# Optimization experiments

Measured on AMD Instinct MI355X. Metric: run time of the kernel, lower is better.

The kernel has to match this reference:

```python
import jax, jax.numpy as jnp
import numpy as np

N_NODES = 50000
N_EDGES = 1600000
NFEAT = 256
NHID = 32
HEADS = 8
NCLASS = 2
NEG_SLOPE = 0.2  # DGL GATConv default


def gat_layer(x, src, dst, W, al, ar, b, num_nodes):
    """DGL-style GATConv layer.
    x: [N, in], W: [in, H*F], al/ar: [H, F], b: [H*F].
    Returns [N, H*F].
    """
    H, F = al.shape
    feat = (x @ W).reshape(num_nodes, H, F)          # [N, H, F]
    el = jnp.einsum('nhf,hf->nh', feat, al)          # [N, H]
    er = jnp.einsum('nhf,hf->nh', feat, ar)          # [N, H]
    e = jax.nn.leaky_relu(el[src] + er[dst], NEG_SLOPE)  # [E, H]
    # segment softmax over incoming edges of each dst node
    m = jax.ops.segment_max(e, dst, num_segments=num_nodes)  # [N, H]
    m = jnp.where(jnp.isfinite(m), m, 0.0)
    m = jax.lax.stop_gradient(m)
    ee = jnp.exp(e - m[dst])                          # [E, H]
    denom = jax.ops.segment_sum(ee, dst, num_segments=num_nodes)  # [N, H]
    alpha = ee / jnp.maximum(denom[dst], 1e-16)       # [E, H]
    # weighted scatter-aggregation of source features
    msg = feat[src] * alpha[:, :, None]               # [E, H, F]
    out = jax.ops.segment_sum(msg, dst, num_segments=num_nodes)  # [N, H, F]
    return out.reshape(num_nodes, H * F) + b


def setup_inputs() -> dict:
    key = jax.random.key(0)
    ks = jax.random.split(key, 10)
    x = jax.random.normal(ks[0], (N_NODES, NFEAT), dtype=jnp.float32)
    edge_src = jax.random.randint(ks[1], (N_EDGES,), 0, N_NODES, dtype=jnp.int32)
    edge_dst = jax.random.randint(ks[2], (N_EDGES,), 0, N_NODES, dtype=jnp.int32)
    s1 = 1.0 / np.sqrt(NFEAT)
    W1 = jax.random.normal(ks[3], (NFEAT, HEADS * NHID), dtype=jnp.float32) * s1
    al1 = jax.random.normal(ks[4], (HEADS, NHID), dtype=jnp.float32) * 0.1
    ar1 = jax.random.normal(ks[5], (HEADS, NHID), dtype=jnp.float32) * 0.1
    b1 = jnp.zeros((HEADS * NHID,), dtype=jnp.float32)
    s2 = 1.0 / np.sqrt(HEADS * NHID)
    W2 = jax.random.normal(ks[6], (HEADS * NHID, NCLASS), dtype=jnp.float32) * s2
    al2 = jax.random.normal(ks[7], (1, NCLASS), dtype=jnp.float32) * 0.1
    ar2 = jax.random.normal(ks[8], (1, NCLASS), dtype=jnp.float32) * 0.1
    b2 = jnp.zeros((NCLASS,), dtype=jnp.float32)
    return {"x": x, "edge_src": edge_src, "edge_dst": edge_dst,
            "W1": W1, "al1": al1, "ar1": ar1, "b1": b1,
            "W2": W2, "al2": al2, "ar2": ar2, "b2": b2}


def reference(x, edge_src, edge_dst, W1, al1, ar1, b1, W2, al2, ar2, b2):
    h = gat_layer(x, edge_src, edge_dst, W1, al1, ar1, b1, N_NODES)  # [N, 8*nhid]
    h = jax.nn.elu(h)
    h = gat_layer(h, edge_src, edge_dst, W2, al2, ar2, b2, N_NODES)  # [N, nclass]
    return jax.nn.log_softmax(h, axis=1)
```

## Files before the change

### kernel.cpp

```cpp
#include <hip/hip_runtime.h>
#include <hip/hip_fp8.h>


#define NN 50000
#define NE 1600000
#define NBK 196
#define NPB 512
#define PCH 3125
#define CAP 16384

typedef __attribute__((ext_vector_type(8))) short short8;
typedef __attribute__((ext_vector_type(4))) float f32x4;
typedef __attribute__((ext_vector_type(2))) float f32x2;

__device__ inline unsigned short f2bf(float f) {
  unsigned int u = __float_as_uint(f);
  unsigned int r = (u + 0x7fffu + ((u >> 16) & 1u)) >> 16;
  return (unsigned short)r;
}
__device__ inline unsigned char f2fp8(float f) {
  __hip_fp8_e4m3 q(f);
  return *reinterpret_cast<unsigned char*>(&q);
}
__device__ inline float lrelu_exp(float v) {
  v = v >= 0.f ? v : 0.2f * v;
  return __expf(v);
}

__global__ __launch_bounds__(256) void k_hist2(const int* __restrict__ dst,
                                               int* __restrict__ hmat) {
  __shared__ int h[NBK];
  int tid = threadIdx.x, blk = blockIdx.x;
  for (int i = tid; i < NBK; i += 256) h[i] = 0;
  __syncthreads();
  int b0 = blk * PCH;
  for (int k = tid; k < PCH; k += 256)
    atomicAdd(&h[dst[b0 + k] >> 8], 1);
  __syncthreads();
  for (int i = tid; i < NBK; i += 256)
    hmat[(size_t)i * NPB + blk] = h[i];
}

__global__ __launch_bounds__(512) void k_cscan(int* __restrict__ hmat,
                                               int* __restrict__ cur) {
  __shared__ int buf[NPB];
  int b = blockIdx.x, tid = threadIdx.x;
  int v = hmat[(size_t)b * NPB + tid];
  buf[tid] = v;
  __syncthreads();
  for (int off = 1; off < NPB; off <<= 1) {
    int t = (tid >= off) ? buf[tid - off] : 0;
    __syncthreads();
    buf[tid] += t;
    __syncthreads();
  }
  hmat[(size_t)b * NPB + tid] = buf[tid] - v;
  if (tid == NPB - 1) cur[b] = buf[tid];
}

__global__ __launch_bounds__(256) void k_bscan(const int* __restrict__ cur,
                                               int* __restrict__ bbase) {
  __shared__ int buf[256];
  int tid = threadIdx.x;
  int v = (tid < NBK) ? cur[tid] : 0;
  buf[tid] = v;
  __syncthreads();
  for (int off = 1; off < 256; off <<= 1) {
    int t = (tid >= off) ? buf[tid - off] : 0;
    __syncthreads();
    buf[tid] += t;
    __syncthreads();
  }
  if (tid < NBK) bbase[tid] = buf[tid] - v;
  if (tid == NBK - 1) bbase[NBK] = buf[tid];
}

__global__ __launch_bounds__(256) void k_part2(const int* __restrict__ dst,
                                               const int* __restrict__ src,
                                               const int* __restrict__ hmat,
                                               int* __restrict__ stage) {
  __shared__ int sbuf[PCH];
  __shared__ int h[NBK], scn[NBK], base[NBK], lofs[NBK];
  __shared__ int sc[256];
  int tid = threadIdx.x, blk = blockIdx.x;
  for (int i = tid; i < NBK; i += 256) { h[i] = 0; lofs[i] = 0; }
  __syncthreads();
  int b0 = blk * PCH;
  for (int k = tid; k < PCH; k += 256)
    atomicAdd(&h[dst[b0 + k] >> 8], 1);
  __syncthreads();
  int v = (tid < NBK) ? h[tid] : 0;
  sc[tid] = v;
  __syncthreads();
  for (int off = 1; off < 256; off <<= 1) {
    int t = (tid >= off) ? sc[tid - off] : 0;
    __syncthreads();
    sc[tid] += t;
    __syncthreads();
  }
  if (tid < NBK) {
    scn[tid] = sc[tid] - v;
    base[tid] = hmat[(size_t)tid * NPB + blk];
  }
  __syncthreads();
  for (int k = tid; k < PCH; k += 256) {
    int i = b0 + k;
    int d = dst[i];
    int b = d >> 8;
    int r = atomicAdd(&lofs[b], 1);
    sbuf[scn[b] + r] = (b << 24) | ((d & 255) << 16) | src[i];
  }
  __syncthreads();
  for (int i = tid; i < PCH; i += 256) {
    int e = sbuf[i];
    int b = (unsigned)e >> 24;
    stage[(size_t)b * CAP + base[b] + (i - scn[b])] = e;
  }
}

__global__ __launch_bounds__(512) void k_build(const int* __restrict__ stage,
                                               const int* __restrict__ bbase,
                                               int* __restrict__ offs,
                                               unsigned short* __restrict__ csr,
                                               int n, int E) {
  __shared__ int h[256], buf[256], cur[256];
  int b = blockIdx.x, tid = threadIdx.x;
  int beg = bbase[b];
  int tot = bbase[b + 1] - beg;
  const int* st = stage + (size_t)b * CAP;
  if (tid < 256) h[tid] = 0;
  __syncthreads();
  for (int k = tid; k < tot; k += 512)
    atomicAdd(&h[(st[k] >> 16) & 255], 1);
  __syncthreads();
  int v = (tid < 256) ? h[tid] : 0;
  if (tid < 256) buf[tid] = v;
  __syncthreads();
  for (int off = 1; off < 256; off <<= 1) {
    int t = (tid >= off && tid < 256) ? buf[tid - off] : 0;
    __syncthreads();
    if (tid < 256) buf[tid] += t;
    __syncthreads();
  }
  if (tid < 256) {
    int excl = buf[tid] - v;
    int node = b * 256 + tid;
    if (node < n) offs[node] = beg + excl;
    cur[tid] = excl;
  }
  if (b == 0 && tid == 0) offs[n] = E;
  __syncthreads();
  for (int k = tid; k < tot; k += 512) {
    int p = st[k];
    int r = atomicAdd(&cur[(p >> 16) & 255], 1);
    csr[beg + r] = (unsigned short)(p & 0xFFFF);
  }
}

__global__ __launch_bounds__(256) void k_packw(const float* __restrict__ W1,
                                               const float* __restrict__ al,
                                               const float* __restrict__ ar,
                                               unsigned short* __restrict__ W1p,
                                               unsigned short* __restrict__ walar) {
  int idx = blockIdx.x * 256 + threadIdx.x;
  if (idx < 8192) {
    int nf = idx >> 9, rem = idx & 511;
    int ks = rem >> 6, lane = rem & 63;
    int n = nf * 16 + (lane & 15);
    int kb = ks * 32 + (lane >> 4) * 8;
#pragma unroll
    for (int j = 0; j < 8; ++j)
      W1p[(size_t)idx * 8 + j] = f2bf(W1[(kb + j) * 256 + n]);
  } else if (idx < 8192 + 512) {
    int idx2 = idx - 8192;
    int ks = idx2 >> 6, lane = idx2 & 63;
    int n = lane & 15;
    int kb = ks * 32 + (lane >> 4) * 8;
    const float* coef = (n < 8) ? (al + n * 32) : (ar + (n - 8) * 32);
    int bc = (n < 8) ? n * 32 : (n - 8) * 32;
#pragma unroll
    for (int j = 0; j < 8; ++j) {
      int k = kb + j;
      float s = 0.f;
      for (int f = 0; f < 32; ++f) s += W1[k * 256 + bc + f] * coef[f];
      walar[(size_t)idx2 * 8 + j] = f2bf(s);
    }
  }
}

__global__ __launch_bounds__(256) void k_gemm1m(
    const float* __restrict__ x, const unsigned short* __restrict__ W1p,
    const unsigned short* __restrict__ walar,
    unsigned char* __restrict__ feat8, float* __restrict__ el,
    float* __restrict__ er, int n) {
  __shared__ unsigned short xs[32][264];
  int w = threadIdx.x >> 6, lane = threadIdx.x & 63;
  int tile = blockIdx.x * 32;
  if (tile >= n) return;
  for (int idx = threadIdx.x; idx < 2048; idx += 256) {
    int r = idx >> 6, c4 = (idx & 63) * 4;
    int row = tile + r;
    float4 v = (row < n)
                   ? *reinterpret_cast<const float4*>(x + (size_t)row * 256 + c4)
                   : make_float4(0.f, 0.f, 0.f, 0.f);
    xs[r][c4 + 0] = f2bf(v.x);
    xs[r][c4 + 1] = f2bf(v.y);
    xs[r][c4 + 2] = f2bf(v.z);
    xs[r][c4 + 3] = f2bf(v.w);
  }
  __syncthreads();
  int r0 = lane & 15, kgrp = lane >> 4;
  int nf0 = w * 4;
  f32x4 acc[4][2];
  f32x4 accE[2];
#pragma unroll
  for (int nf = 0; nf < 4; ++nf)
#pragma unroll
    for (int mf = 0; mf < 2; ++mf) acc[nf][mf] = (f32x4){0.f, 0.f, 0.f, 0.f};
  accE[0] = (f32x4){0.f, 0.f, 0.f, 0.f};
  accE[1] = (f32x4){0.f, 0.f, 0.f, 0.f};

  for (int ks = 0; ks < 8; ++ks) {
    int kb = ks * 32 + kgrp * 8;
    short8 a0 = *reinterpret_cast<const short8*>(&xs[r0][kb]);
    short8 a1 = *reinterpret_cast<const short8*>(&xs[16 + r0][kb]);
#pragma unroll
    for (int nf = 0; nf < 4; ++nf) {
      short8 b = *reinterpret_cast<const short8*>(
          W1p + ((size_t)((nf0 + nf) * 8 + ks) * 64 + lane) * 8);
      acc[nf][0] = __builtin_amdgcn_mfma_f32_16x16x32_bf16(a0, b, acc[nf][0], 0, 0, 0);
      acc[nf][1] = __builtin_amdgcn_mfma_f32_16x16x32_bf16(a1, b, acc[nf][1], 0, 0, 0);
    }
    if (w == 0) {
      short8 bE = *reinterpret_cast<const short8*>(
          walar + ((size_t)ks * 64 + lane) * 8);
      accE[0] = __builtin_amdgcn_mfma_f32_16x16x32_bf16(a0, bE, accE[0], 0, 0, 0);
      accE[1] = __builtin_amdgcn_mfma_f32_16x16x32_bf16(a1, bE, accE[1], 0, 0, 0);
    }
  }
#pragma unroll
  for (int nf = 0; nf < 4; ++nf)
#pragma unroll
    for (int mf = 0; mf < 2; ++mf)
#pragma unroll
      for (int q = 0; q < 4; ++q) {
        int row = tile + mf * 16 + kgrp * 4 + q;
        if (row < n)
          feat8[(size_t)row * 256 + (nf0 + nf) * 16 + r0] = f2fp8(acc[nf][mf][q]);
      }
  if (w == 0) {
#pragma unroll
    for (int mf = 0; mf < 2; ++mf)
#pragma unroll
      for (int q = 0; q < 4; ++q) {
        int row = tile + mf * 16 + kgrp * 4 + q;
        if (row < n) {
          if (r0 < 8) el[(size_t)row * 8 + r0] = accE[mf][q];
          else        er[(size_t)row * 8 + (r0 - 8)] = accE[mf][q];
        }
      }
  }
}

__global__ __launch_bounds__(256) void k_agg1(
    const unsigned char* __restrict__ feat8, const float* __restrict__ el,
    const float* __restrict__ er, const int* __restrict__ offs,
    const unsigned short* __restrict__ csr, const float* __restrict__ b1,
    const float* __restrict__ W2, const float* __restrict__ al2,
    const float* __restrict__ ar2, float4* __restrict__ node4, int n) {
  int dn = blockIdx.x * 4 + (threadIdx.x >> 6);
  if (dn >= n) return;
  int l = threadIdx.x & 63;
  int hh = l >> 3;
  int h8 = l & 7;
  float erv = er[dn * 8 + h8];
  int beg = offs[dn], end = offs[dn + 1];
  f32x2 acc01 = {0.f, 0.f}, acc23 = {0.f, 0.f};
  float den = 0.f;
  int g = beg;
  for (; g + 8 <= end; g += 8) {
    int s_my = csr[g + (l >> 3)];
    float eev = lrelu_exp(el[s_my * 8 + h8] + erv);
#pragma unroll
    for (int e = 0; e < 8; ++e) {
      int s = __builtin_amdgcn_readlane(s_my, e * 8);
      float ee = __shfl(eev, e * 8 + hh, 64);
      den += ee;
      const unsigned char* rowp = feat8 + (size_t)s * 256;
      unsigned int fv = *reinterpret_cast<const unsigned int*>(rowp + l * 4);
      f32x2 lo = __builtin_amdgcn_cvt_pk_f32_fp8(fv, false);
      f32x2 hi = __builtin_amdgcn_cvt_pk_f32_fp8(fv, true);
      f32x2 ee2 = {ee, ee};
      acc01 = ee2 * lo + acc01;
      acc23 = ee2 * hi + acc23;
    }
  }
  if (g < end) {
    int rem = end - g;
    int idx = g + (l >> 3);
    int s_t = csr[idx < end ? idx : end - 1];
    float ee_t = lrelu_exp(el[s_t * 8 + h8] + erv);
    for (int e = 0; e < rem; ++e) {
      int s = __builtin_amdgcn_readlane(s_t, e * 8);
      float ee = __shfl(ee_t, e * 8 + hh, 64);
      den += ee;
      const unsigned char* rowp = feat8 + (size_t)s * 256;
      unsigned int fv = *reinterpret_cast<const unsigned int*>(rowp + l * 4);
      f32x2 lo = __builtin_amdgcn_cvt_pk_f32_fp8(fv, false);
      f32x2 hi = __builtin_amdgcn_cvt_pk_f32_fp8(fv, true);
      f32x2 ee2 = {ee, ee};
      acc01 = ee2 * lo + acc01;
      acc23 = ee2 * hi + acc23;
    }
  }
  float4 bv = *reinterpret_cast<const float4*>(b1 + l * 4);
  float4 w2e = *reinterpret_cast<const float4*>(W2 + l * 8);
  float4 w2o = *reinterpret_cast<const float4*>(W2 + l * 8 + 4);
  float inv = 1.f / fmaxf(den, 1e-16f);
  float v0 = acc01[0] * inv + bv.x; v0 = v0 > 0.f ? v0 : expm1f(v0);
  float v1 = acc01[1] * inv + bv.y; v1 = v1 > 0.f ? v1 : expm1f(v1);
  float v2 = acc23[0] * inv + bv.z; v2 = v2 > 0.f ? v2 : expm1f(v2);
  float v3 = acc23[1] * inv + bv.w; v3 = v3 > 0.f ? v3 : expm1f(v3);
  float p0 = v0 * w2e.x + v1 * w2e.z + v2 * w2o.x + v3 * w2o.z;
  float p1 = v0 * w2e.y + v1 * w2e.w + v2 * w2o.y + v3 * w2o.w;
#pragma unroll
  for (int off = 32; off; off >>= 1) {
    p0 += __shfl_xor(p0, off, 64);
    p1 += __shfl_xor(p1, off, 64);
  }
  if (l == 0) {
    float e2 = p0 * al2[0] + p1 * al2[1];
    float r2 = p0 * ar2[0] + p1 * ar2[1];
    node4[dn] = make_float4(p0, p1, e2, r2);
  }
}

__global__ __launch_bounds__(256) void k_agg2(
    const float4* __restrict__ node4, const int* __restrict__ offs,
    const unsigned short* __restrict__ csr, const float* __restrict__ b2,
    float* __restrict__ out, int n) {
  int dn = blockIdx.x * 4 + (threadIdx.x >> 6);
  int l = threadIdx.x & 63;
  if (dn >= n) return;
  float erd = node4[dn].w;
  int beg = offs[dn], end = offs[dn + 1];
  float den = 0.f, a0 = 0.f, a1 = 0.f;
  for (int e = beg + l; e < end; e += 64) {
    int s = csr[e];
    float4 n4 = node4[s];
    float ev = n4.z + erd;
    ev = ev >= 0.f ? ev : 0.2f * ev;
    float ee = __expf(ev);
    den += ee;
    a0 = fmaf(ee, n4.x, a0);
    a1 = fmaf(ee, n4.y, a1);
  }
#pragma unroll
  for (int off = 32; off; off >>= 1) {
    den += __shfl_xor(den, off, 64);
    a0 += __shfl_xor(a0, off, 64);
    a1 += __shfl_xor(a1, off, 64);
  }
  if (l == 0) {
    float inv = 1.f / fmaxf(den, 1e-16f);
    float z0 = a0 * inv + b2[0];
    float z1 = a1 * inv + b2[1];
    float m = fmaxf(z0, z1);
    float lse = m + logf(__expf(z0 - m) + __expf(z1 - m));
    out[dn * 2 + 0] = z0 - lse;
    out[dn * 2 + 1] = z1 - lse;
  }
}

extern "C" void kernel_launch(void* const* d_in, const int* in_sizes, int n_in,
                              void* d_out, int out_size, void* d_ws,
                              size_t ws_size, hipStream_t stream) {
  const float* x   = (const float*)d_in[0];
  const int* esrc  = (const int*)d_in[1];
  const int* edst  = (const int*)d_in[2];
  const float* W1  = (const float*)d_in[3];
  const float* al1 = (const float*)d_in[4];
  const float* ar1 = (const float*)d_in[5];
  const float* b1  = (const float*)d_in[6];
  const float* W2  = (const float*)d_in[7];
  const float* al2 = (const float*)d_in[8];
  const float* ar2 = (const float*)d_in[9];
  const float* b2  = (const float*)d_in[10];
  float* out = (float*)d_out;

  size_t off = 0;
  auto alloc = [&](size_t bytes) {
    void* p = (char*)d_ws + off;
    off += (bytes + 255) & ~(size_t)255;
    return p;
  };
  unsigned char* feat8 = (unsigned char*)alloc((size_t)NN * 256);
  unsigned short* W1p  = (unsigned short*)alloc((size_t)16 * 8 * 64 * 8 * 2);
  unsigned short* walar = (unsigned short*)alloc((size_t)8 * 64 * 8 * 2);
  float* el1    = (float*)alloc((size_t)NN * 8 * 4);
  float* er1    = (float*)alloc((size_t)NN * 8 * 4);
  float4* node4 = (float4*)alloc((size_t)NN * 16);
  int* stage    = (int*)alloc((size_t)NBK * CAP * 4);
  int* hmat     = (int*)alloc((size_t)NBK * NPB * 4);
  unsigned short* csr = (unsigned short*)alloc((size_t)NE * 2);
  int* offs     = (int*)alloc((size_t)(NN + 1) * 4);
  int* cur      = (int*)alloc((size_t)NBK * 4);
  int* bbase    = (int*)alloc((size_t)(NBK + 1) * 4);

  k_hist2<<<NPB, 256, 0, stream>>>(edst, hmat);
  k_cscan<<<NBK, NPB, 0, stream>>>(hmat, cur);
  k_bscan<<<1, 256, 0, stream>>>(cur, bbase);
  k_part2<<<NPB, 256, 0, stream>>>(edst, esrc, hmat, stage);
  k_build<<<NBK, 512, 0, stream>>>(stage, bbase, offs, csr, NN, NE);

  k_packw<<<34, 256, 0, stream>>>(W1, al1, ar1, W1p, walar);
  k_gemm1m<<<(NN + 31) / 32, 256, 0, stream>>>(x, W1p, walar, feat8, el1,
                                               er1, NN);
  k_agg1<<<(NN + 3) / 4, 256, 0, stream>>>(feat8, el1, er1, offs, csr, b1, W2,
                                           al2, ar2, node4, NN);
  k_agg2<<<(NN + 3) / 4, 256, 0, stream>>>(node4, offs, csr, b2, out, NN);
}
```

Measured before the change: 163.1 us.

## Drop global bucket scan by using padded per-bucket CSR with degree array

Removes the single-block bucket prefix scan kernel by laying out the CSR in fixed-capacity per-bucket slots and storing per-node degree alongside offsets. The partition kernel caches dst values in shared memory to avoid reading them twice from global memory. The second aggregation kernel now uses 32 lanes per destination node instead of 64, matching the low average degree. The padded CSR enlarges the buffer and adds a degree load per node.

```diff
diff --git a/kernel.cpp b/kernel.cpp
--- a/kernel.cpp
+++ b/kernel.cpp
@@ -58,36 +58,23 @@
   if (tid == NPB - 1) cur[b] = buf[tid];
 }
 
-__global__ __launch_bounds__(256) void k_bscan(const int* __restrict__ cur,
-                                               int* __restrict__ bbase) {
-  __shared__ int buf[256];
-  int tid = threadIdx.x;
-  int v = (tid < NBK) ? cur[tid] : 0;
-  buf[tid] = v;
-  __syncthreads();
-  for (int off = 1; off < 256; off <<= 1) {
-    int t = (tid >= off) ? buf[tid - off] : 0;
-    __syncthreads();
-    buf[tid] += t;
-    __syncthreads();
-  }
-  if (tid < NBK) bbase[tid] = buf[tid] - v;
-  if (tid == NBK - 1) bbase[NBK] = buf[tid];
-}
-
 __global__ __launch_bounds__(256) void k_part2(const int* __restrict__ dst,
                                                const int* __restrict__ src,
                                                const int* __restrict__ hmat,
                                                int* __restrict__ stage) {
   __shared__ int sbuf[PCH];
+  __shared__ int dbuf[PCH];
   __shared__ int h[NBK], scn[NBK], base[NBK], lofs[NBK];
   __shared__ int sc[256];
   int tid = threadIdx.x, blk = blockIdx.x;
   for (int i = tid; i < NBK; i += 256) { h[i] = 0; lofs[i] = 0; }
   __syncthreads();
   int b0 = blk * PCH;
-  for (int k = tid; k < PCH; k += 256)
-    atomicAdd(&h[dst[b0 + k] >> 8], 1);
+  for (int k = tid; k < PCH; k += 256) {
+    int d = dst[b0 + k];
+    dbuf[k] = d;
+    atomicAdd(&h[d >> 8], 1);
+  }
   __syncthreads();
   int v = (tid < NBK) ? h[tid] : 0;
   sc[tid] = v;
@@ -104,11 +91,10 @@
   }
   __syncthreads();
   for (int k = tid; k < PCH; k += 256) {
-    int i = b0 + k;
-    int d = dst[i];
+    int d = dbuf[k];
     int b = d >> 8;
     int r = atomicAdd(&lofs[b], 1);
-    sbuf[scn[b] + r] = (b << 24) | ((d & 255) << 16) | src[i];
+    sbuf[scn[b] + r] = (b << 24) | ((d & 255) << 16) | src[b0 + k];
   }
   __syncthreads();
   for (int i = tid; i < PCH; i += 256) {
@@ -119,15 +105,16 @@
 }
 
 __global__ __launch_bounds__(512) void k_build(const int* __restrict__ stage,
-                                               const int* __restrict__ bbase,
+                                               const int* __restrict__ tots,
                                                int* __restrict__ offs,
+                                               int* __restrict__ deg,
                                                unsigned short* __restrict__ csr,
-                                               int n, int E) {
+                                               int n) {
   __shared__ int h[256], buf[256], cur[256];
   int b = blockIdx.x, tid = threadIdx.x;
-  int beg = bbase[b];
-  int tot = bbase[b + 1] - beg;
+  int tot = tots[b];
   const int* st = stage + (size_t)b * CAP;
+  unsigned short* cs = csr + (size_t)b * CAP;
   if (tid < 256) h[tid] = 0;
   __syncthreads();
   for (int k = tid; k < tot; k += 512)
@@ -145,15 +132,17 @@
   if (tid < 256) {
     int excl = buf[tid] - v;
     int node = b * 256 + tid;
-    if (node < n) offs[node] = beg + excl;
+    if (node < n) {
+      offs[node] = b * CAP + excl;
+      deg[node] = v;
+    }
     cur[tid] = excl;
   }
-  if (b == 0 && tid == 0) offs[n] = E;
   __syncthreads();
   for (int k = tid; k < tot; k += 512) {
     int p = st[k];
     int r = atomicAdd(&cur[(p >> 16) & 255], 1);
-    csr[beg + r] = (unsigned short)(p & 0xFFFF);
+    cs[r] = (unsigned short)(p & 0xFFFF);
   }
 }
 
@@ -265,16 +254,17 @@
 __global__ __launch_bounds__(256) void k_agg1(
     const unsigned char* __restrict__ feat8, const float* __restrict__ el,
     const float* __restrict__ er, const int* __restrict__ offs,
-    const unsigned short* __restrict__ csr, const float* __restrict__ b1,
-    const float* __restrict__ W2, const float* __restrict__ al2,
-    const float* __restrict__ ar2, float4* __restrict__ node4, int n) {
+    const int* __restrict__ deg, const unsigned short* __restrict__ csr,
+    const float* __restrict__ b1, const float* __restrict__ W2,
+    const float* __restrict__ al2, const float* __restrict__ ar2,
+    float4* __restrict__ node4, int n) {
   int dn = blockIdx.x * 4 + (threadIdx.x >> 6);
   if (dn >= n) return;
   int l = threadIdx.x & 63;
   int hh = l >> 3;
   int h8 = l & 7;
   float erv = er[dn * 8 + h8];
-  int beg = offs[dn], end = offs[dn + 1];
+  int beg = offs[dn], end = beg + deg[dn];
   f32x2 acc01 = {0.f, 0.f}, acc23 = {0.f, 0.f};
   float den = 0.f;
   int g = beg;
@@ -337,15 +327,15 @@
 
 __global__ __launch_bounds__(256) void k_agg2(
     const float4* __restrict__ node4, const int* __restrict__ offs,
-    const unsigned short* __restrict__ csr, const float* __restrict__ b2,
-    float* __restrict__ out, int n) {
-  int dn = blockIdx.x * 4 + (threadIdx.x >> 6);
-  int l = threadIdx.x & 63;
+    const int* __restrict__ deg, const unsigned short* __restrict__ csr,
+    const float* __restrict__ b2, float* __restrict__ out, int n) {
+  int dn = blockIdx.x * 8 + (threadIdx.x >> 5);
+  int l = threadIdx.x & 31;
   if (dn >= n) return;
   float erd = node4[dn].w;
-  int beg = offs[dn], end = offs[dn + 1];
+  int beg = offs[dn], end = beg + deg[dn];
   float den = 0.f, a0 = 0.f, a1 = 0.f;
-  for (int e = beg + l; e < end; e += 64) {
+  for (int e = beg + l; e < end; e += 32) {
     int s = csr[e];
     float4 n4 = node4[s];
     float ev = n4.z + erd;
@@ -356,10 +346,10 @@
     a1 = fmaf(ee, n4.y, a1);
   }
 #pragma unroll
-  for (int off = 32; off; off >>= 1) {
-    den += __shfl_xor(den, off, 64);
-    a0 += __shfl_xor(a0, off, 64);
-    a1 += __shfl_xor(a1, off, 64);
+  for (int off = 16; off; off >>= 1) {
+    den += __shfl_xor(den, off, 32);
+    a0 += __shfl_xor(a0, off, 32);
+    a1 += __shfl_xor(a1, off, 32);
   }
   if (l == 0) {
     float inv = 1.f / fmaxf(den, 1e-16f);
@@ -402,21 +392,20 @@
   float4* node4 = (float4*)alloc((size_t)NN * 16);
   int* stage    = (int*)alloc((size_t)NBK * CAP * 4);
   int* hmat     = (int*)alloc((size_t)NBK * NPB * 4);
-  unsigned short* csr = (unsigned short*)alloc((size_t)NE * 2);
-  int* offs     = (int*)alloc((size_t)(NN + 1) * 4);
+  unsigned short* csr = (unsigned short*)alloc((size_t)NBK * CAP * 2);
+  int* offs     = (int*)alloc((size_t)NN * 4);
+  int* deg      = (int*)alloc((size_t)NN * 4);
   int* cur      = (int*)alloc((size_t)NBK * 4);
-  int* bbase    = (int*)alloc((size_t)(NBK + 1) * 4);
 
   k_hist2<<<NPB, 256, 0, stream>>>(edst, hmat);
   k_cscan<<<NBK, NPB, 0, stream>>>(hmat, cur);
-  k_bscan<<<1, 256, 0, stream>>>(cur, bbase);
   k_part2<<<NPB, 256, 0, stream>>>(edst, esrc, hmat, stage);
-  k_build<<<NBK, 512, 0, stream>>>(stage, bbase, offs, csr, NN, NE);
+  k_build<<<NBK, 512, 0, stream>>>(stage, cur, offs, deg, csr, NN);
 
   k_packw<<<34, 256, 0, stream>>>(W1, al1, ar1, W1p, walar);
   k_gemm1m<<<(NN + 31) / 32, 256, 0, stream>>>(x, W1p, walar, feat8, el1,
                                                er1, NN);
-  k_agg1<<<(NN + 3) / 4, 256, 0, stream>>>(feat8, el1, er1, offs, csr, b1, W2,
-                                           al2, ar2, node4, NN);
-  k_agg2<<<(NN + 3) / 4, 256, 0, stream>>>(node4, offs, csr, b2, out, NN);
-}
+  k_agg1<<<(NN + 3) / 4, 256, 0, stream>>>(feat8, el1, er1, offs, deg, csr, b1,
+                                           W2, al2, ar2, node4, NN);
+  k_agg2<<<(NN + 7) / 8, 256, 0, stream>>>(node4, offs, deg, csr, b2, out, NN);
+}
```

Measured after the change: 159.7 us. 1.02x faster.
